# Kernel optimization log

Hardware: AMD Instinct MI355X
Metric: run time of the kernel (lower is better)

The kernel has to match this reference:

```python
import jax, jax.numpy as jnp
import numpy as np
from jax import lax

N_HEADS = 12
HEAD_DIM = 64
ALPHA = 4.0  # spikingjelly surrogate.Sigmoid default alpha
EPS = 1e-5   # BatchNorm1d default eps

@jax.custom_vjp
def _heaviside(v):
    return (v >= 0.0).astype(v.dtype)

def _heaviside_fwd(v):
    return _heaviside(v), v

def _heaviside_bwd(v, g):
    sg = jax.nn.sigmoid(ALPHA * v)
    return (g * ALPHA * sg * (1.0 - sg),)

_heaviside.defvjp(_heaviside_fwd, _heaviside_bwd)

def if_node(x):
    """Multi-step IFNode (v_threshold=1, hard reset to 0), scan over leading T dim."""
    def step(v, xt):
        v = v + xt                      # integrate
        s = _heaviside(v - 1.0)         # fire
        v = (1.0 - s) * v               # hard reset: spiked neurons -> 0
        return v, s
    _, spikes = lax.scan(step, jnp.zeros_like(x[0]), x)
    return spikes

def bn1d(x):
    """Fresh (training-mode) BatchNorm1d over (T, S, D) with channels=S;
    affine weight=1, bias=0 at init, so pure normalization over axes (0,2)."""
    mean = x.mean(axis=(0, 2), keepdims=True)
    var = x.var(axis=(0, 2), keepdims=True)  # biased variance, as torch BN uses
    return (x - mean) * lax.rsqrt(var + EPS)

def setup_inputs() -> dict:
    key = jax.random.key(0)
    ks = jax.random.split(key, 5)
    T, S, D = 4, 2048, 768
    x = jax.random.normal(ks[0], (T, S, D), dtype=jnp.float32)
    scale = 0.02
    wq = jax.random.normal(ks[1], (D, D), dtype=jnp.float32) * scale
    wk = jax.random.normal(ks[2], (D, D), dtype=jnp.float32) * scale
    wv = jax.random.normal(ks[3], (D, D), dtype=jnp.float32) * scale
    wo = jax.random.normal(ks[4], (D, D), dtype=jnp.float32) * scale
    return {"x": x, "wq": wq, "wk": wk, "wv": wv, "wo": wo, "cur_pos": S}

def reference(x, wq, wk, wv, wo, cur_pos):
    T, S, D = x.shape
    tmp = if_node(x)                    # init_spike
    Q = tmp @ wq
    V = tmp @ wv
    K = tmp @ wk
    Q = if_node(bn1d(Q))                # spike_q(bnq(Q))
    V = if_node(bn1d(V))                # spike_v(bnv(V))
    K = if_node(bn1d(K))                # spike_k(bnk(K))
    # (T, S, H, hd) -> (T, H, S, hd)
    Qh = Q.reshape(T, S, N_HEADS, HEAD_DIM).transpose(0, 2, 1, 3)
    Vh = V.reshape(T, S, N_HEADS, HEAD_DIM).transpose(0, 2, 1, 3)
    Kh = K.reshape(T, S, N_HEADS, HEAD_DIM).transpose(0, 2, 1, 3)
    QK = (Qh * Kh).sum(axis=2, keepdims=True)   # (T, H, 1, hd)
    QK = if_node(QK)                    # talking_heads
    QKV = Vh * QK                       # (T, H, S, hd)
    QKV = QKV.transpose(0, 2, 1, 3).reshape(T, S, D)
    return bn1d(QKV @ wo)
```

## Files before the change

kernel.cpp:

```cpp
#include <hip/hip_runtime.h>

#define T_ 4
#define S_ 2048
#define D_ 768
#define SD_ (S_ * D_)
#define TSD_ (T_ * SD_)
#define H_ 12
#define HD_ 64
#define PLANE_BYTES 2359296u

typedef int int32x4 __attribute__((ext_vector_type(4)));

__device__ __forceinline__ void cp16(unsigned char* lds, const unsigned char* g) {
    __builtin_amdgcn_global_load_lds(
        (const __attribute__((address_space(1))) unsigned int*)g,
        (__attribute__((address_space(3))) unsigned int*)lds, 16, 0, 0);
}

__device__ __forceinline__ size_t frag_addr(int m, int d) {
    return ((size_t)(m >> 4) * 12 + (d >> 6)) * 1024 +
           (size_t)(((d >> 4) & 3) * 256 + (m & 15) * 16 + (d & 15));
}

__global__ __launch_bounds__(256) void k_prep_all(const float* __restrict__ wq,
                                                  const float* __restrict__ wk,
                                                  const float* __restrict__ wv,
                                                  const float* __restrict__ wo,
                                                  const float* __restrict__ x,
                                                  unsigned char* __restrict__ Bp,
                                                  unsigned char* __restrict__ Sx,
                                                  unsigned int* __restrict__ QKp) {
    __shared__ unsigned char wl[4096];
    int tid = threadIdx.x;
    if (blockIdx.y < 4) {
        const float* W = (blockIdx.y == 0) ? wq : (blockIdx.y == 1) ? wk
                       : (blockIdx.y == 2) ? wv : wo;
        unsigned char* out = Bp + (size_t)blockIdx.y * PLANE_BYTES;
        int c = blockIdx.x;
        int kb = c % 12;
        int nbg = c / 12;
        int k_loc = tid >> 2;
        int n_base = (tid & 3) * 4;
        float4 w4 = *(const float4*)(
            W + (size_t)(kb * 64 + k_loc) * D_ + nbg * 16 + n_base);
        float wsv[4] = {w4.x, w4.y, w4.z, w4.w};
#pragma unroll
        for (int j = 0; j < 4; j++) {
            int n_loc = n_base + j;
            int u = (int)rintf(wsv[j] * 1073741824.0f);
#pragma unroll
            for (int p = 0; p < 4; p++) {
                wl[p * 1024 + (n_loc + 16 * (k_loc >> 4)) * 16 + (k_loc & 15)] =
                    (unsigned char)(u & 255);
                u = (u + 128) >> 8;
            }
        }
        __syncthreads();
        int p = tid >> 6;
        int lane = tid & 63;
        uint4 val = *(const uint4*)&wl[p * 1024 + lane * 16];
        *(uint4*)(out + (size_t)((p * 48 + nbg) * 12 + kb) * 1024 + lane * 16) =
            val;
    } else {
        if (blockIdx.x >= 384) {
            if (blockIdx.x < 432) {
                int idx = (blockIdx.x - 384) * 256 + tid;
                QKp[idx] = 0u;
            }
            return;
        }
        int gid = blockIdx.x * 256 + tid;
        int s = gid / 48;
        int d0 = (gid % 48) * 16;
        double v[16];
#pragma unroll
        for (int j = 0; j < 16; j++) v[j] = 0.0;
#pragma unroll
        for (int t = 0; t < T_; t++) {
            union { uint4 u; unsigned char b[16]; } sp;
#pragma unroll
            for (int q = 0; q < 4; q++) {
                float4 xt = *(const float4*)(
                    x + (size_t)t * SD_ + (size_t)s * D_ + d0 + q * 4);
                float xs[4] = {xt.x, xt.y, xt.z, xt.w};
#pragma unroll
                for (int j = 0; j < 4; j++) {
                    int jj = q * 4 + j;
                    v[jj] += (double)xs[j];
                    unsigned char ss = (v[jj] >= 1.0) ? 1 : 0;
                    sp.b[jj] = ss;
                    if (ss) v[jj] = 0.0;
                }
            }
            *(uint4*)(Sx + frag_addr(t * S_ + s, d0)) = sp.u;
        }
    }
}

__global__ __launch_bounds__(256, 2) void k_gemm_i8(
    const unsigned char* __restrict__ A,
    const unsigned char* __restrict__ Bp,
    const unsigned int* __restrict__ Mp,
    float* __restrict__ C0, float* __restrict__ C1, float* __restrict__ C2,
    int bzoff) {
    int z = blockIdx.z;
    const unsigned char* B = Bp + (size_t)(bzoff + z) * PLANE_BYTES;
    float* C = (z == 0) ? C0 : (z == 1) ? C1 : C2;

    __shared__ __align__(16) unsigned char bsm[2 * 32768];
    __shared__ __align__(16) unsigned int maskw[192];

    int tid = threadIdx.x;
    int lane = tid & 63;
    int w = tid >> 6;
    int wm = w >> 1;
    int wn = w & 1;
    int row0 = blockIdx.x * 128;
    int tI = row0 >> 11;
    int n0 = blockIdx.y * 64;
    int nbg0 = blockIdx.y * 4;
    int col = lane & 15;
    int quad = lane >> 4;

    int32x4 zerov = {0, 0, 0, 0};
    int32x4 acc[4][2][4];
#pragma unroll
    for (int mb = 0; mb < 4; mb++)
#pragma unroll
        for (int nb = 0; nb < 2; nb++)
#pragma unroll
            for (int p = 0; p < 4; p++) acc[mb][nb][p] = zerov;

    const unsigned char* Ab =
        A + (size_t)((row0 >> 4) + wm * 4) * 12 * 1024 + lane * 16;

    auto stageB = [&](int buf, int kb2) {
        unsigned char* bb = bsm + buf * 32768;
#pragma unroll
        for (int kk = 0; kk < 2; kk++)
#pragma unroll
            for (int qi = 0; qi < 4; qi++) {
                int q = w * 4 + qi;
                int p = q >> 2, nb = q & 3;
                cp16(bb + kk * 16384 + q * 1024,
                     B + (size_t)((p * 48 + nbg0 + nb) * 12 + 2 * kb2 + kk) *
                             1024 + lane * 16);
            }
    };

    stageB(0, 0);
    if (Mp && tid < 192) {
        unsigned int m = 0;
#pragma unroll
        for (int c = 0; c < 16; c++) m |= Mp[c * 768 + tI * 192 + tid];
        maskw[tid] = m;
    }
    int32x4 a[2][4];
#pragma unroll
    for (int mb = 0; mb < 4; mb++)
        a[0][mb] = *(const int32x4*)(Ab + (size_t)(mb * 12) * 1024);
    __syncthreads();

    for (int kb2 = 0; kb2 < 6; kb2++) {
        int cur = kb2 & 1;
        if (kb2 < 5) stageB(1 - cur, kb2 + 1);
#pragma unroll
        for (int kbh = 0; kbh < 2; kbh++) {
            int kb = kb2 * 2 + kbh;
            if (kb < 11) {
#pragma unroll
                for (int mb = 0; mb < 4; mb++)
                    a[(kb + 1) & 1][mb] = *(const int32x4*)(
                        Ab + (size_t)(mb * 12 + kb + 1) * 1024);
            }
            int32x4 af[4];
#pragma unroll
            for (int mb = 0; mb < 4; mb++) af[mb] = a[kb & 1][mb];
            if (Mp) {
                int32x4 mv = *(const int32x4*)(
                    (const unsigned char*)maskw + kb * 64 + quad * 16);
#pragma unroll
                for (int mb = 0; mb < 4; mb++) af[mb] &= mv;
            }
            const unsigned char* bb = bsm + cur * 32768 + kbh * 16384;
#pragma unroll
            for (int p = 0; p < 4; p++)
#pragma unroll
                for (int nb = 0; nb < 2; nb++) {
                    int32x4 bf = *(const int32x4*)(
                        bb + (size_t)(p * 4 + wn * 2 + nb) * 1024 + lane * 16);
#pragma unroll
                    for (int mb = 0; mb < 4; mb++)
                        acc[mb][nb][p] = __builtin_amdgcn_mfma_i32_16x16x64_i8(
                            af[mb], bf, acc[mb][nb][p], 0, 0, 0);
                }
        }
        __syncthreads();
    }

#pragma unroll
    for (int mb = 0; mb < 4; mb++)
#pragma unroll
        for (int nb = 0; nb < 2; nb++)
#pragma unroll
            for (int r = 0; r < 4; r++) {
                double td = (double)acc[mb][nb][0][r]
                          + 256.0 * (double)acc[mb][nb][1][r]
                          + 65536.0 * (double)acc[mb][nb][2][r]
                          + 16777216.0 * (double)acc[mb][nb][3][r];
                float v = (float)(td * (1.0 / 1073741824.0));
                int rr = row0 + wm * 64 + mb * 16 + quad * 4 + r;
                int cc = n0 + wn * 32 + nb * 16 + col;
                C[(size_t)rr * D_ + cc] = v;
            }
}

__global__ __launch_bounds__(256) void k_bnif_qk(const float* __restrict__ Qf,
                                                 const float* __restrict__ Kf,
                                                 const float* __restrict__ Vf,
                                                 unsigned char* __restrict__ Vs,
                                                 unsigned int* __restrict__ QKp) {
    int s = blockIdx.x;
    __shared__ float buf[3][T_][D_];
    __shared__ double red[4][6];
    __shared__ unsigned char spkV[T_ * D_];
    __shared__ unsigned char spkA[T_ * D_];
    __shared__ double stats[3][2];

    int tid = threadIdx.x;
    int lane = tid & 63, wv = tid >> 6;
    const float* Xs[3] = {Qf, Kf, Vf};
    double sum[3] = {0.0, 0.0, 0.0}, sumsq[3] = {0.0, 0.0, 0.0};
#pragma unroll
    for (int y = 0; y < 3; y++) {
#pragma unroll
        for (int i = 0; i < 3; i++) {
            int idx = i * 256 + tid;
            int t = idx / 192;
            int c = idx - t * 192;
            float4 v = *(const float4*)(
                Xs[y] + (size_t)t * SD_ + (size_t)s * D_ + c * 4);
            *(float4*)&buf[y][t][c * 4] = v;
            sum[y] += ((double)v.x + (double)v.y) +
                      ((double)v.z + (double)v.w);
            sumsq[y] += ((double)v.x * v.x + (double)v.y * v.y) +
                        ((double)v.z * v.z + (double)v.w * v.w);
        }
    }
#pragma unroll
    for (int off = 32; off > 0; off >>= 1) {
#pragma unroll
        for (int y = 0; y < 3; y++) {
            sum[y] += __shfl_down(sum[y], off);
            sumsq[y] += __shfl_down(sumsq[y], off);
        }
    }
    if (lane == 0) {
#pragma unroll
        for (int y = 0; y < 3; y++) {
            red[wv][y] = sum[y];
            red[wv][3 + y] = sumsq[y];
        }
    }
    __syncthreads();
    if (tid < 3) {
        double s4 = red[0][tid] + red[1][tid] + red[2][tid] + red[3][tid];
        double q4 = red[0][3 + tid] + red[1][3 + tid] + red[2][3 + tid] +
                    red[3][3 + tid];
        double mean = s4 / 3072.0;
        double var = q4 / 3072.0 - mean * mean;
        stats[tid][0] = mean;
        stats[tid][1] = 1.0 / sqrt(var + 1e-5);
    }
    __syncthreads();

    for (int d = tid; d < D_; d += 256) {
        unsigned char qs[T_], ks[T_];
#pragma unroll
        for (int y = 0; y < 3; y++) {
            double mean = stats[y][0], rstd = stats[y][1];
            double v = 0.0;
#pragma unroll
            for (int t = 0; t < T_; t++) {
                double xn = ((double)buf[y][t][d] - mean) * rstd;
                v += xn;
                unsigned char sp = (v >= 1.0) ? 1 : 0;
                if (y == 0) qs[t] = sp;
                else if (y == 1) ks[t] = sp;
                else spkV[t * D_ + d] = sp;
                if (sp) v = 0.0;
            }
        }
#pragma unroll
        for (int t = 0; t < T_; t++) spkA[t * D_ + d] = qs[t] & ks[t];
    }
    __syncthreads();

    if (tid < 192) {
        int tt = tid / 48, gg = tid % 48;
        uint4 val = *(const uint4*)&spkV[tt * D_ + gg * 16];
        size_t dst = ((size_t)(tt * 128 + (s >> 4)) * 12 + (gg >> 2)) * 1024 +
                     (size_t)((gg & 3) * 256 + (s & 15) * 16);
        *(uint4*)(Vs + dst) = val;
        unsigned int* dstq = QKp + (s & 15) * 768;
#pragma unroll
        for (int t = 0; t < T_; t++) {
            unsigned int word = *(const unsigned int*)&spkA[t * D_ + tid * 4];
            if (word) atomicOr(dstq + t * 192 + tid, word);
        }
    }
}

__global__ __launch_bounds__(256) void k_bn_out(const float* __restrict__ Xin,
                                                float* __restrict__ out) {
    int s = blockIdx.x;
    __shared__ double red[4][2];
    __shared__ double st[2];
    int tid = threadIdx.x;
    int lane = tid & 63, wv = tid >> 6;
    float4 vv[3];
    double sum = 0.0, sumsq = 0.0;
#pragma unroll
    for (int i = 0; i < 3; i++) {
        int idx = i * 256 + tid;
        int t = idx / 192, c = idx - t * 192;
        float4 v = *(const float4*)(
            Xin + (size_t)t * SD_ + (size_t)s * D_ + c * 4);
        vv[i] = v;
        sum += ((double)v.x + (double)v.y) + ((double)v.z + (double)v.w);
        sumsq += ((double)v.x * v.x + (double)v.y * v.y) +
                 ((double)v.z * v.z + (double)v.w * v.w);
    }
#pragma unroll
    for (int off = 32; off > 0; off >>= 1) {
        sum += __shfl_down(sum, off);
        sumsq += __shfl_down(sumsq, off);
    }
    if (lane == 0) { red[wv][0] = sum; red[wv][1] = sumsq; }
    __syncthreads();
    if (tid == 0) {
        double s4 = red[0][0] + red[1][0] + red[2][0] + red[3][0];
        double q4 = red[0][1] + red[1][1] + red[2][1] + red[3][1];
        double mean = s4 / 3072.0;
        double var = q4 / 3072.0 - mean * mean;
        st[0] = mean;
        st[1] = 1.0 / sqrt(var + 1e-5);
    }
    __syncthreads();
    double mean = st[0], rstd = st[1];
#pragma unroll
    for (int i = 0; i < 3; i++) {
        int idx = i * 256 + tid;
        int t = idx / 192, c = idx - t * 192;
        float4 o;
        o.x = (float)(((double)vv[i].x - mean) * rstd);
        o.y = (float)(((double)vv[i].y - mean) * rstd);
        o.z = (float)(((double)vv[i].z - mean) * rstd);
        o.w = (float)(((double)vv[i].w - mean) * rstd);
        *(float4*)(out + (size_t)t * SD_ + (size_t)s * D_ + c * 4) = o;
    }
}

extern "C" void kernel_launch(void* const* d_in, const int* in_sizes, int n_in,
                              void* d_out, int out_size, void* d_ws,
                              size_t ws_size, hipStream_t stream) {
    const float* x  = (const float*)d_in[0];
    const float* wq = (const float*)d_in[1];
    const float* wk = (const float*)d_in[2];
    const float* wv = (const float*)d_in[3];
    const float* wo = (const float*)d_in[4];
    float* out = (float*)d_out;

    float* ws  = (float*)d_ws;
    float* Qf  = ws;
    float* Kf  = ws + (size_t)TSD_;
    float* Vf  = ws + (size_t)2 * TSD_;
    unsigned int* QKp = (unsigned int*)(ws + (size_t)3 * TSD_);
    unsigned char* Sx = (unsigned char*)(QKp + 12288);
    unsigned char* Vs = Sx + (size_t)TSD_;
    unsigned char* Bp = Vs + (size_t)TSD_;

    k_prep_all<<<dim3(576, 5), 256, 0, stream>>>(wq, wk, wv, wo, x, Bp, Sx,
                                                 QKp);
    k_gemm_i8<<<dim3(64, 12, 3), 256, 0, stream>>>(Sx, Bp, nullptr,
                                                   Qf, Kf, Vf, 0);
    k_bnif_qk<<<S_, 256, 0, stream>>>(Qf, Kf, Vf, Vs, QKp);
    k_gemm_i8<<<dim3(64, 12, 1), 256, 0, stream>>>(Vs, Bp, QKp, Qf, Qf, Qf, 3);
    k_bn_out<<<S_, 256, 0, stream>>>(Qf, out);
}
```

Before: 200.0 us.

## Stage input spikes through LDS and pack QK mask via wave ballots

The input spike prep now has each block handle 16 rows. It stages the spike bytes in padded shared memory and then writes whole 16-row fragment tiles contiguously, replacing the earlier scattered 16-byte stores. The QK talking-heads mask is built with wave ballots into 64-bit bitmasks, using atomicOr from one lane per wave instead of per-byte shared arrays and many 32-bit atomics. The GEMM unpacks these bitmask words back into byte-lane masks. The cost is larger shared memory in the prep kernel, fewer prep blocks, and extra bit-manipulation in the GEMM prologue.

Result: no change. 202.8 us (+1.4%).

```diff
diff --git a/kernel.cpp b/kernel.cpp
--- a/kernel.cpp
+++ b/kernel.cpp
@@ -30,9 +30,10 @@
                                                   unsigned char* __restrict__ Bp,
                                                   unsigned char* __restrict__ Sx,
                                                   unsigned int* __restrict__ QKp) {
-    __shared__ unsigned char wl[4096];
+    __shared__ __align__(16) unsigned char shm[50176];
     int tid = threadIdx.x;
     if (blockIdx.y < 4) {
+        unsigned char* wl = shm;
         const float* W = (blockIdx.y == 0) ? wq : (blockIdx.y == 1) ? wk
                        : (blockIdx.y == 2) ? wv : wo;
         unsigned char* out = Bp + (size_t)blockIdx.y * PLANE_BYTES;
@@ -62,37 +63,54 @@
         *(uint4*)(out + (size_t)((p * 48 + nbg) * 12 + kb) * 1024 + lane * 16) =
             val;
     } else {
-        if (blockIdx.x >= 384) {
-            if (blockIdx.x < 432) {
-                int idx = (blockIdx.x - 384) * 256 + tid;
-                QKp[idx] = 0u;
+        if (blockIdx.x >= 128) {
+            if (blockIdx.x == 128) {
+                for (int i = tid; i < 1536; i += 256) QKp[i] = 0u;
             }
             return;
         }
-        int gid = blockIdx.x * 256 + tid;
-        int s = gid / 48;
-        int d0 = (gid % 48) * 16;
-        double v[16];
-#pragma unroll
-        for (int j = 0; j < 16; j++) v[j] = 0.0;
-#pragma unroll
-        for (int t = 0; t < T_; t++) {
-            union { uint4 u; unsigned char b[16]; } sp;
-#pragma unroll
-            for (int q = 0; q < 4; q++) {
-                float4 xt = *(const float4*)(
-                    x + (size_t)t * SD_ + (size_t)s * D_ + d0 + q * 4);
-                float xs[4] = {xt.x, xt.y, xt.z, xt.w};
-#pragma unroll
-                for (int j = 0; j < 4; j++) {
-                    int jj = q * 4 + j;
-                    v[jj] += (double)xs[j];
-                    unsigned char ss = (v[jj] >= 1.0) ? 1 : 0;
-                    sp.b[jj] = ss;
-                    if (ss) v[jj] = 0.0;
+        int s0 = blockIdx.x * 16;
+        uint4* sx = (uint4*)shm;
+        for (int p = 0; p < 3; p++) {
+            int pi = tid + p * 256;
+            int sl = pi / 48;
+            int dc = pi % 48;
+            int d0 = dc * 16;
+            double v[16];
+#pragma unroll
+            for (int j = 0; j < 16; j++) v[j] = 0.0;
+#pragma unroll
+            for (int t = 0; t < T_; t++) {
+                union { uint4 u; unsigned char b[16]; } sp;
+#pragma unroll
+                for (int q = 0; q < 4; q++) {
+                    float4 xt = *(const float4*)(
+                        x + (size_t)t * SD_ + (size_t)(s0 + sl) * D_ + d0 +
+                        q * 4);
+                    float xs[4] = {xt.x, xt.y, xt.z, xt.w};
+#pragma unroll
+                    for (int j = 0; j < 4; j++) {
+                        int jj = q * 4 + j;
+                        v[jj] += (double)xs[j];
+                        unsigned char ss = (v[jj] >= 1.0) ? 1 : 0;
+                        sp.b[jj] = ss;
+                        if (ss) v[jj] = 0.0;
+                    }
                 }
-            }
-            *(uint4*)(Sx + frag_addr(t * S_ + s, d0)) = sp.u;
+                sx[(t * 16 + sl) * 49 + dc] = sp.u;
+            }
+        }
+        __syncthreads();
+#pragma unroll
+        for (int j = 0; j < 12; j++) {
+            int f = tid + j * 256;
+            int t = f / 768;
+            int u = f % 768;
+            int sl = u & 15;
+            int dc = ((u >> 6) << 2) | ((u >> 4) & 3);
+            uint4 val = sx[(t * 16 + sl) * 49 + dc];
+            *(uint4*)(Sx + ((size_t)(t * 128 + (s0 >> 4)) * 12) * 1024 +
+                      (size_t)u * 16) = val;
         }
     }
 }
@@ -150,10 +168,14 @@
 
     stageB(0, 0);
     if (Mp && tid < 192) {
-        unsigned int m = 0;
-#pragma unroll
-        for (int c = 0; c < 16; c++) m |= Mp[c * 768 + tI * 192 + tid];
-        maskw[tid] = m;
+        const unsigned long long* Qb = (const unsigned long long*)Mp;
+        unsigned long long m = 0;
+#pragma unroll
+        for (int c = 0; c < 16; c++) m |= Qb[(c * 4 + tI) * 12 + (tid >> 4)];
+        unsigned int nib =
+            (unsigned int)((m >> (4 * (tid & 15))) & 0xFull);
+        maskw[tid] = (nib & 1u) | ((nib & 2u) << 7) | ((nib & 4u) << 14) |
+                     ((nib & 8u) << 21);
     }
     int32x4 a[2][4];
 #pragma unroll
@@ -224,7 +246,6 @@
     __shared__ float buf[3][T_][D_];
     __shared__ double red[4][6];
     __shared__ unsigned char spkV[T_ * D_];
-    __shared__ unsigned char spkA[T_ * D_];
     __shared__ double stats[3][2];
 
     int tid = threadIdx.x;
@@ -274,7 +295,11 @@
     }
     __syncthreads();
 
-    for (int d = tid; d < D_; d += 256) {
+    unsigned long long* QKb =
+        (unsigned long long*)QKp + ((size_t)(s & 15) * 4) * 12;
+#pragma unroll
+    for (int i = 0; i < 3; i++) {
+        int d = i * 256 + tid;
         unsigned char qs[T_], ks[T_];
 #pragma unroll
         for (int y = 0; y < 3; y++) {
@@ -292,7 +317,10 @@
             }
         }
 #pragma unroll
-        for (int t = 0; t < T_; t++) spkA[t * D_ + d] = qs[t] & ks[t];
+        for (int t = 0; t < T_; t++) {
+            unsigned long long b = __ballot(qs[t] & ks[t]);
+            if (lane == 0 && b) atomicOr(QKb + t * 12 + (i * 4 + wv), b);
+        }
     }
     __syncthreads();
 
@@ -302,12 +330,6 @@
         size_t dst = ((size_t)(tt * 128 + (s >> 4)) * 12 + (gg >> 2)) * 1024 +
                      (size_t)((gg & 3) * 256 + (s & 15) * 16);
         *(uint4*)(Vs + dst) = val;
-        unsigned int* dstq = QKp + (s & 15) * 768;
-#pragma unroll
-        for (int t = 0; t < T_; t++) {
-            unsigned int word = *(const unsigned int*)&spkA[t * D_ + tid * 4];
-            if (word) atomicOr(dstq + t * 192 + tid, word);
-        }
     }
 }
 
```

## Fuse all five kernels into a persistent megakernel with grid barriers

Applied to the files above, without the earlier changes.

Replaces the five separate launches (prep, QKV int8 GEMM, BN+IF+QK, output GEMM, output BN) with a single persistent kernel of 512 blocks. The blocks loop over virtual block indices for each phase and are separated by atomic-counter grid barriers. The aim is to remove per-launch overhead and the idle gaps between kernels. The cost is that every phase now runs on a fixed grid with one shared LDS allocation, occupancy may drop for the phases that needed less LDS, and correctness depends on all 512 blocks being co-resident.

Result: slower. 489.7 us (+144.8%).

```diff
diff --git a/kernel.cpp b/kernel.cpp
--- a/kernel.cpp
+++ b/kernel.cpp
@@ -8,6 +8,7 @@
 #define H_ 12
 #define HD_ 64
 #define PLANE_BYTES 2359296u
+#define GRID_N 512
 
 typedef int int32x4 __attribute__((ext_vector_type(4)));
 
@@ -22,21 +23,34 @@
            (size_t)(((d >> 4) & 3) * 256 + (m & 15) * 16 + (d & 15));
 }
 
-__global__ __launch_bounds__(256) void k_prep_all(const float* __restrict__ wq,
-                                                  const float* __restrict__ wk,
-                                                  const float* __restrict__ wv,
-                                                  const float* __restrict__ wo,
-                                                  const float* __restrict__ x,
-                                                  unsigned char* __restrict__ Bp,
-                                                  unsigned char* __restrict__ Sx,
-                                                  unsigned int* __restrict__ QKp) {
-    __shared__ unsigned char wl[4096];
+__device__ __forceinline__ void gbar(unsigned int* cnt, unsigned int target) {
+    __syncthreads();
+    if (threadIdx.x == 0) {
+        __threadfence();
+        atomicAdd(cnt, 1u);
+        int guard = 0;
+        while (atomicAdd(cnt, 0u) < target && guard < (1 << 24)) {
+            __builtin_amdgcn_s_sleep(2);
+            guard++;
+        }
+        __threadfence();
+    }
+    __syncthreads();
+}
+
+__device__ __forceinline__ void phase_prep(
+    int vb, const float* __restrict__ wq, const float* __restrict__ wk,
+    const float* __restrict__ wv, const float* __restrict__ wo,
+    const float* __restrict__ x, unsigned char* __restrict__ Bp,
+    unsigned char* __restrict__ Sx, unsigned int* __restrict__ QKp,
+    unsigned char* smem) {
     int tid = threadIdx.x;
-    if (blockIdx.y < 4) {
-        const float* W = (blockIdx.y == 0) ? wq : (blockIdx.y == 1) ? wk
-                       : (blockIdx.y == 2) ? wv : wo;
-        unsigned char* out = Bp + (size_t)blockIdx.y * PLANE_BYTES;
-        int c = blockIdx.x;
+    if (vb < 2304) {
+        unsigned char* wl = smem;
+        int wy = vb / 576;
+        const float* W = (wy == 0) ? wq : (wy == 1) ? wk : (wy == 2) ? wv : wo;
+        unsigned char* out = Bp + (size_t)wy * PLANE_BYTES;
+        int c = vb % 576;
         int kb = c % 12;
         int nbg = c / 12;
         int k_loc = tid >> 2;
@@ -61,15 +75,9 @@
         uint4 val = *(const uint4*)&wl[p * 1024 + lane * 16];
         *(uint4*)(out + (size_t)((p * 48 + nbg) * 12 + kb) * 1024 + lane * 16) =
             val;
-    } else {
-        if (blockIdx.x >= 384) {
-            if (blockIdx.x < 432) {
-                int idx = (blockIdx.x - 384) * 256 + tid;
-                QKp[idx] = 0u;
-            }
-            return;
-        }
-        int gid = blockIdx.x * 256 + tid;
+        __syncthreads();
+    } else if (vb < 2688) {
+        int gid = (vb - 2304) * 256 + tid;
         int s = gid / 48;
         int d0 = (gid % 48) * 16;
         double v[16];
@@ -94,31 +102,28 @@
             }
             *(uint4*)(Sx + frag_addr(t * S_ + s, d0)) = sp.u;
         }
-    }
-}
-
-__global__ __launch_bounds__(256, 2) void k_gemm_i8(
-    const unsigned char* __restrict__ A,
-    const unsigned char* __restrict__ Bp,
-    const unsigned int* __restrict__ Mp,
-    float* __restrict__ C0, float* __restrict__ C1, float* __restrict__ C2,
-    int bzoff) {
-    int z = blockIdx.z;
-    const unsigned char* B = Bp + (size_t)(bzoff + z) * PLANE_BYTES;
-    float* C = (z == 0) ? C0 : (z == 1) ? C1 : C2;
-
-    __shared__ __align__(16) unsigned char bsm[2 * 32768];
-    __shared__ __align__(16) unsigned int maskw[192];
+    } else {
+        int idx = (vb - 2688) * 256 + tid;
+        if (idx < 12288) QKp[idx] = 0u;
+    }
+}
+
+__device__ __forceinline__ void phase_gemm(
+    const unsigned char* __restrict__ A, const unsigned char* __restrict__ B,
+    const unsigned int* __restrict__ Mp, float* __restrict__ C,
+    int bx, int by, unsigned char* smem) {
+    unsigned char* bsm = smem;
+    unsigned int* maskw = (unsigned int*)(smem + 65536);
 
     int tid = threadIdx.x;
     int lane = tid & 63;
     int w = tid >> 6;
     int wm = w >> 1;
     int wn = w & 1;
-    int row0 = blockIdx.x * 128;
+    int row0 = bx * 128;
     int tI = row0 >> 11;
-    int n0 = blockIdx.y * 64;
-    int nbg0 = blockIdx.y * 4;
+    int n0 = by * 64;
+    int nbg0 = by * 4;
     int col = lane & 15;
     int quad = lane >> 4;
 
@@ -215,17 +220,15 @@
             }
 }
 
-__global__ __launch_bounds__(256) void k_bnif_qk(const float* __restrict__ Qf,
-                                                 const float* __restrict__ Kf,
-                                                 const float* __restrict__ Vf,
-                                                 unsigned char* __restrict__ Vs,
-                                                 unsigned int* __restrict__ QKp) {
-    int s = blockIdx.x;
-    __shared__ float buf[3][T_][D_];
-    __shared__ double red[4][6];
-    __shared__ unsigned char spkV[T_ * D_];
-    __shared__ unsigned char spkA[T_ * D_];
-    __shared__ double stats[3][2];
+__device__ __forceinline__ void phase_bnif(
+    int s, const float* __restrict__ Qf, const float* __restrict__ Kf,
+    const float* __restrict__ Vf, unsigned char* __restrict__ Vs,
+    unsigned int* __restrict__ QKp, unsigned char* smem) {
+    float (*buf)[T_][D_] = (float (*)[T_][D_])smem;
+    unsigned char* spkV = smem + 36864;
+    unsigned char* spkA = smem + 39936;
+    double (*red)[6] = (double (*)[6])(smem + 43008);
+    double (*stats)[2] = (double (*)[2])(smem + 43200);
 
     int tid = threadIdx.x;
     int lane = tid & 63, wv = tid >> 6;
@@ -311,11 +314,10 @@
     }
 }
 
-__global__ __launch_bounds__(256) void k_bn_out(const float* __restrict__ Xin,
-                                                float* __restrict__ out) {
-    int s = blockIdx.x;
-    __shared__ double red[4][2];
-    __shared__ double st[2];
+__device__ __forceinline__ void phase_bnout(
+    int s, const float* __restrict__ Xin, float* __restrict__ out,
+    unsigned char* smem) {
+    double* red = (double*)smem;
     int tid = threadIdx.x;
     int lane = tid & 63, wv = tid >> 6;
     float4 vv[3];
@@ -336,18 +338,19 @@
         sum += __shfl_down(sum, off);
         sumsq += __shfl_down(sumsq, off);
     }
-    if (lane == 0) { red[wv][0] = sum; red[wv][1] = sumsq; }
+    __syncthreads();
+    if (lane == 0) { red[wv * 2] = sum; red[wv * 2 + 1] = sumsq; }
     __syncthreads();
     if (tid == 0) {
-        double s4 = red[0][0] + red[1][0] + red[2][0] + red[3][0];
-        double q4 = red[0][1] + red[1][1] + red[2][1] + red[3][1];
+        double s4 = red[0] + red[2] + red[4] + red[6];
+        double q4 = red[1] + red[3] + red[5] + red[7];
         double mean = s4 / 3072.0;
         double var = q4 / 3072.0 - mean * mean;
-        st[0] = mean;
-        st[1] = 1.0 / sqrt(var + 1e-5);
-    }
-    __syncthreads();
-    double mean = st[0], rstd = st[1];
+        red[8] = mean;
+        red[9] = 1.0 / sqrt(var + 1e-5);
+    }
+    __syncthreads();
+    double mean = red[8], rstd = red[9];
 #pragma unroll
     for (int i = 0; i < 3; i++) {
         int idx = i * 256 + tid;
@@ -361,6 +364,42 @@
     }
 }
 
+__global__ __launch_bounds__(256, 2) void k_mega(
+    const float* __restrict__ x, const float* __restrict__ wq,
+    const float* __restrict__ wk, const float* __restrict__ wv,
+    const float* __restrict__ wo, float* __restrict__ out,
+    float* __restrict__ Qf, float* __restrict__ Kf, float* __restrict__ Vf,
+    unsigned int* __restrict__ QKp, unsigned char* __restrict__ Sx,
+    unsigned char* __restrict__ Vs, unsigned char* __restrict__ Bp,
+    unsigned int* __restrict__ bar) {
+    __shared__ __align__(16) unsigned char smem[66560];
+    int bid = blockIdx.x;
+
+    for (int vb = bid; vb < 2736; vb += GRID_N)
+        phase_prep(vb, wq, wk, wv, wo, x, Bp, Sx, QKp, smem);
+    gbar(bar, 1 * GRID_N);
+
+    for (int vb = bid; vb < 2304; vb += GRID_N) {
+        int z = vb / 768, r = vb % 768;
+        float* C = (z == 0) ? Qf : (z == 1) ? Kf : Vf;
+        phase_gemm(Sx, Bp + (size_t)z * PLANE_BYTES, nullptr, C,
+                   r & 63, r >> 6, smem);
+    }
+    gbar(bar, 2 * GRID_N);
+
+    for (int vb = bid; vb < 2048; vb += GRID_N)
+        phase_bnif(vb, Qf, Kf, Vf, Vs, QKp, smem);
+    gbar(bar, 3 * GRID_N);
+
+    for (int vb = bid; vb < 768; vb += GRID_N)
+        phase_gemm(Vs, Bp + (size_t)3 * PLANE_BYTES, QKp, Qf,
+                   vb & 63, vb >> 6, smem);
+    gbar(bar, 4 * GRID_N);
+
+    for (int vb = bid; vb < 2048; vb += GRID_N)
+        phase_bnout(vb, Qf, out, smem);
+}
+
 extern "C" void kernel_launch(void* const* d_in, const int* in_sizes, int n_in,
                               void* d_out, int out_size, void* d_ws,
                               size_t ws_size, hipStream_t stream) {
@@ -379,12 +418,9 @@
     unsigned char* Sx = (unsigned char*)(QKp + 12288);
     unsigned char* Vs = Sx + (size_t)TSD_;
     unsigned char* Bp = Vs + (size_t)TSD_;
-
-    k_prep_all<<<dim3(576, 5), 256, 0, stream>>>(wq, wk, wv, wo, x, Bp, Sx,
-                                                 QKp);
-    k_gemm_i8<<<dim3(64, 12, 3), 256, 0, stream>>>(Sx, Bp, nullptr,
-                                                   Qf, Kf, Vf, 0);
-    k_bnif_qk<<<S_, 256, 0, stream>>>(Qf, Kf, Vf, Vs, QKp);
-    k_gemm_i8<<<dim3(64, 12, 1), 256, 0, stream>>>(Vs, Bp, QKp, Qf, Qf, Qf, 3);
-    k_bn_out<<<S_, 256, 0, stream>>>(Qf, out);
-}
+    unsigned int* bar = (unsigned int*)(Bp + (size_t)4 * PLANE_BYTES);
+
+    hipMemsetAsync(bar, 0, 64, stream);
+    k_mega<<<GRID_N, 256, 0, stream>>>(x, wq, wk, wv, wo, out,
+                                       Qf, Kf, Vf, QKp, Sx, Vs, Bp, bar);
+}
```

## Load GEMM B fragments directly from global memory instead of LDS staging

Applied to the files above, without the earlier changes.

The int8 GEMM kernel stops staging B tiles into double-buffered shared memory with async global-to-LDS copies. Each warp now reads its B fragments straight from global memory into registers, and the per-iteration block barriers are removed. This frees 64KB of LDS per block and drops the sync overhead, which could allow higher occupancy. In exchange, B data is no longer shared across the two row-warps, so global and L2 traffic increases, and load latency is no longer hidden by the prefetch pipeline.

New measurement: 245.5 us. +22.7%, slower.

```diff
diff --git a/kernel.cpp b/kernel.cpp
--- a/kernel.cpp
+++ b/kernel.cpp
@@ -10,12 +10,6 @@
 #define PLANE_BYTES 2359296u
 
 typedef int int32x4 __attribute__((ext_vector_type(4)));
-
-__device__ __forceinline__ void cp16(unsigned char* lds, const unsigned char* g) {
-    __builtin_amdgcn_global_load_lds(
-        (const __attribute__((address_space(1))) unsigned int*)g,
-        (__attribute__((address_space(3))) unsigned int*)lds, 16, 0, 0);
-}
 
 __device__ __forceinline__ size_t frag_addr(int m, int d) {
     return ((size_t)(m >> 4) * 12 + (d >> 6)) * 1024 +
@@ -107,7 +101,6 @@
     const unsigned char* B = Bp + (size_t)(bzoff + z) * PLANE_BYTES;
     float* C = (z == 0) ? C0 : (z == 1) ? C1 : C2;
 
-    __shared__ __align__(16) unsigned char bsm[2 * 32768];
     __shared__ __align__(16) unsigned int maskw[192];
 
     int tid = threadIdx.x;
@@ -133,69 +126,49 @@
 
     const unsigned char* Ab =
         A + (size_t)((row0 >> 4) + wm * 4) * 12 * 1024 + lane * 16;
-
-    auto stageB = [&](int buf, int kb2) {
-        unsigned char* bb = bsm + buf * 32768;
-#pragma unroll
-        for (int kk = 0; kk < 2; kk++)
-#pragma unroll
-            for (int qi = 0; qi < 4; qi++) {
-                int q = w * 4 + qi;
-                int p = q >> 2, nb = q & 3;
-                cp16(bb + kk * 16384 + q * 1024,
-                     B + (size_t)((p * 48 + nbg0 + nb) * 12 + 2 * kb2 + kk) *
-                             1024 + lane * 16);
-            }
-    };
-
-    stageB(0, 0);
+    const unsigned char* Bw =
+        B + (size_t)(nbg0 + wn * 2) * 12 * 1024 + lane * 16;
+
     if (Mp && tid < 192) {
         unsigned int m = 0;
 #pragma unroll
         for (int c = 0; c < 16; c++) m |= Mp[c * 768 + tI * 192 + tid];
         maskw[tid] = m;
     }
+    if (Mp) __syncthreads();
+
     int32x4 a[2][4];
 #pragma unroll
     for (int mb = 0; mb < 4; mb++)
         a[0][mb] = *(const int32x4*)(Ab + (size_t)(mb * 12) * 1024);
-    __syncthreads();
-
-    for (int kb2 = 0; kb2 < 6; kb2++) {
-        int cur = kb2 & 1;
-        if (kb2 < 5) stageB(1 - cur, kb2 + 1);
-#pragma unroll
-        for (int kbh = 0; kbh < 2; kbh++) {
-            int kb = kb2 * 2 + kbh;
-            if (kb < 11) {
+
+    for (int kb = 0; kb < 12; kb++) {
+        if (kb < 11) {
+#pragma unroll
+            for (int mb = 0; mb < 4; mb++)
+                a[(kb + 1) & 1][mb] = *(const int32x4*)(
+                    Ab + (size_t)(mb * 12 + kb + 1) * 1024);
+        }
+        int32x4 af[4];
+#pragma unroll
+        for (int mb = 0; mb < 4; mb++) af[mb] = a[kb & 1][mb];
+        if (Mp) {
+            int32x4 mv = *(const int32x4*)(
+                (const unsigned char*)maskw + kb * 64 + quad * 16);
+#pragma unroll
+            for (int mb = 0; mb < 4; mb++) af[mb] &= mv;
+        }
+#pragma unroll
+        for (int p = 0; p < 4; p++)
+#pragma unroll
+            for (int nb = 0; nb < 2; nb++) {
+                int32x4 bf = *(const int32x4*)(
+                    Bw + (size_t)((p * 48 + nb) * 12 + kb) * 1024);
 #pragma unroll
                 for (int mb = 0; mb < 4; mb++)
-                    a[(kb + 1) & 1][mb] = *(const int32x4*)(
-                        Ab + (size_t)(mb * 12 + kb + 1) * 1024);
-            }
-            int32x4 af[4];
-#pragma unroll
-            for (int mb = 0; mb < 4; mb++) af[mb] = a[kb & 1][mb];
-            if (Mp) {
-                int32x4 mv = *(const int32x4*)(
-                    (const unsigned char*)maskw + kb * 64 + quad * 16);
-#pragma unroll
-                for (int mb = 0; mb < 4; mb++) af[mb] &= mv;
-            }
-            const unsigned char* bb = bsm + cur * 32768 + kbh * 16384;
-#pragma unroll
-            for (int p = 0; p < 4; p++)
-#pragma unroll
-                for (int nb = 0; nb < 2; nb++) {
-                    int32x4 bf = *(const int32x4*)(
-                        bb + (size_t)(p * 4 + wn * 2 + nb) * 1024 + lane * 16);
-#pragma unroll
-                    for (int mb = 0; mb < 4; mb++)
-                        acc[mb][nb][p] = __builtin_amdgcn_mfma_i32_16x16x64_i8(
-                            af[mb], bf, acc[mb][nb][p], 0, 0, 0);
-                }
-        }
-        __syncthreads();
+                    acc[mb][nb][p] = __builtin_amdgcn_mfma_i32_16x16x64_i8(
+                        af[mb], bf, acc[mb][nb][p], 0, 0, 0);
+            }
     }
 
 #pragma unroll
```
